# Kernel tuning notes

Hardware: AMD Instinct MI355X
Metric: run time of the kernel (lower is better)

The kernel has to match this reference:

```python
import jax, jax.numpy as jnp
import numpy as np

V, E, M, L = 32000, 1024, 4096, 4  # vocab, embed_dim, mlp_dim, mlp_layers
B, S = 4, 2048                      # batch, seq_len


def setup_inputs() -> dict:
    key = jax.random.key(0)
    ks = jax.random.split(key, 7)
    init = lambda k, shape, fan: (jax.random.normal(k, shape, jnp.float32) / np.sqrt(fan).astype(np.float32))
    return {
        "x": jax.random.randint(ks[0], (B, S), 0, V),
        "emb": init(ks[1], (V, E), E),
        "Wq": init(ks[2], (E, E), E), "bq": jnp.zeros((E,), jnp.float32),
        "Wk": init(ks[3], (E, E), E), "bk": jnp.zeros((E,), jnp.float32),
        "Wv": init(ks[4], (E, E), E), "bv": jnp.zeros((E,), jnp.float32),
        "W1": init(ks[5], (L, E, M), E), "b1": jnp.zeros((L, M), jnp.float32),
        "W2": init(ks[6], (L, M, E), M), "b2": jnp.zeros((L, E), jnp.float32),
    }


def reference(x, emb, Wq, bq, Wk, bk, Wv, bv, W1, b1, W2, b2):
    h = emb[x]                                   # [B,S,E]
    q = h @ Wq + bq
    k = h @ Wk + bk
    v = h @ Wv + bv
    scale = 1.0 / np.sqrt(E).astype(np.float32)
    scores = jnp.einsum("bse,bte->bst", q, k) * scale   # [B,S,S]
    # torch.triu(ones, diagonal=0): keep upper triangle incl. diagonal (anti-causal/suffix mask)
    mask = jnp.triu(jnp.ones((S, S), dtype=bool), k=0)
    scores = jnp.where(mask, scores, -jnp.inf)
    w = jax.nn.softmax(scores, axis=-1)
    h = jax.nn.relu(jnp.einsum("bst,bte->bse", w, v))
    for i in range(L):
        h = jax.nn.relu(h @ W1[i] + b1[i])
        h = jax.nn.relu(h @ W2[i] + b2[i])
    return h
```

## Files before the change

### kernel.cpp

```cpp
#include <hip/hip_runtime.h>
#include <hip/hip_bf16.h>

#define EDIM 1024
#define MDIM 4096
#define SEQ  2048
#define NB   4
#define ROWS 8192

#define BM 128
#define BN 128

typedef short bh8 __attribute__((ext_vector_type(8)));
typedef float f32x16 __attribute__((ext_vector_type(16)));

__device__ __forceinline__ float bf2f(unsigned short u) {
    return __uint_as_float(((unsigned int)u) << 16);
}
__device__ __forceinline__ unsigned short f2bf(float f) {
    unsigned int u = __float_as_uint(f);
    u += 0x7FFFu + ((u >> 16) & 1u);
    return (unsigned short)(u >> 16);
}
__device__ __forceinline__ void splitf(float v, unsigned short& h, unsigned short& l) {
    h = f2bf(v);
    l = f2bf(v - __uint_as_float(((unsigned int)h) << 16));
}
__device__ __forceinline__ void ld4f(const float* __restrict__ p, float* d) {
    const float4 v = *reinterpret_cast<const float4*>(p);
    d[0] = v.x; d[1] = v.y; d[2] = v.z; d[3] = v.w;
}
__device__ __forceinline__ void ld4h(const unsigned short* __restrict__ p, float* d) {
    const ushort4 v = *reinterpret_cast<const ushort4*>(p);
    d[0] = bf2f(v.x); d[1] = bf2f(v.y); d[2] = bf2f(v.z); d[3] = bf2f(v.w);
}

__device__ __forceinline__ void async_copy16(void* lds, const void* g) {
    __builtin_amdgcn_global_load_lds(
        (const __attribute__((address_space(1))) unsigned int*)g,
        (__attribute__((address_space(3))) unsigned int*)lds, 16, 0, 0);
}

__device__ __forceinline__ long long tidx8(int n, int k, int KD16) {
    return ((((long long)(n >> 5) * KD16 + (k >> 4)) * 2 + ((k >> 3) & 1)) * 32 + (n & 31)) * 8;
}

__device__ __forceinline__ void awrite(unsigned short* __restrict__ A, long long rc,
                                       int r, int k, unsigned short h, unsigned short l) {
    const int sub = (k & 31) >> 3, kb = k & 7, rx = r & 7;
    A[rc + ((sub ^ rx) << 3) + kb] = h;
    A[rc + (((4 + sub) ^ rx) << 3) + kb] = l;
}

__global__ __launch_bounds__(64)
void sniff_k(const unsigned int* __restrict__ w, int* __restrict__ flag) {
    int ok = 0;
    const int base = threadIdx.x * 32;
#pragma unroll
    for (int i = 0; i < 32; ++i) {
        const unsigned int v = w[base + i];
        const unsigned int lo = v & 0xFFFFu, hi = v >> 16;
        const unsigned int el = (lo >> 7) & 0xFF, eh = (hi >> 7) & 0xFF;
        const bool okl = (lo == 0u) || (el >= 0x30u && el <= 0x7Eu);
        const bool okh = (hi == 0u) || (eh >= 0x30u && eh <= 0x7Eu);
        ok += (okl && okh) ? 1 : 0;
    }
#pragma unroll
    for (int off = 32; off > 0; off >>= 1) ok += __shfl_down(ok, off);
    if (threadIdx.x == 0) *flag = (ok > 1400) ? 1 : 0;
}

__global__ __launch_bounds__(256)
void gather_k(const int* __restrict__ x, const void* __restrict__ emb,
              unsigned short* __restrict__ hA, const int* __restrict__ flagp) {
    const int bf = *flagp;
    const int row = blockIdx.x;
    const int idx = x[row];
    const int k = threadIdx.x * 4;
    const long long off = (long long)idx * EDIM + k;
    float d[4];
    if (bf) ld4h((const unsigned short*)emb + off, d);
    else    ld4f((const float*)emb + off, d);
    unsigned short h0, l0, h1, l1, h2, l2, h3, l3;
    splitf(d[0], h0, l0); splitf(d[1], h1, l1);
    splitf(d[2], h2, l2); splitf(d[3], h3, l3);
    const int rx = row & 7, sub = (k & 31) >> 3, kb = k & 7;
    const long long rc = ((long long)row * 32 + (k >> 5)) * 64;
    *reinterpret_cast<ushort4*>(hA + rc + ((sub ^ rx) << 3) + kb) = make_ushort4(h0, h1, h2, h3);
    *reinterpret_cast<ushort4*>(hA + rc + (((4 + sub) ^ rx) << 3) + kb) = make_ushort4(l0, l1, l2, l3);
}

__global__ __launch_bounds__(256)
void splitT_tiled_k(const void* __restrict__ in, unsigned short* __restrict__ oh,
                    unsigned short* __restrict__ ol, int Kd, int Nd,
                    long long inOff, const int* __restrict__ flagp, int bF) {
    const int bf = bF ? *flagp : 0;
    const int k0 = blockIdx.y * 32, n0 = blockIdx.x * 32;
    const int KD16 = Kd >> 4;
    __shared__ float t[32][33];
    const int c = threadIdx.x & 31, r0 = threadIdx.x >> 5;
#pragma unroll
    for (int i = 0; i < 4; ++i) {
        const int r = r0 + i * 8;
        const long long off = inOff + (long long)(k0 + r) * Nd + n0 + c;
        t[r][c] = bf ? bf2f(((const unsigned short*)in)[off]) : ((const float*)in)[off];
    }
    __syncthreads();
#pragma unroll
    for (int i = 0; i < 4; ++i) {
        const int r = r0 + i * 8;
        const float v = t[c][r];
        unsigned short hh, ll;
        splitf(v, hh, ll);
        const int n = n0 + r, k = k0 + c;
        const long long oo = tidx8(n, k, KD16) + (k & 7);
        oh[oo] = hh; ol[oo] = ll;
    }
}

template<int OM, bool BIAS, bool RELU, bool MASK>
__global__ __launch_bounds__(256, 3)
void mgemm_k(const unsigned short* __restrict__ A,
             const unsigned short* __restrict__ Bh,
             const unsigned short* __restrict__ Bl,
             const void* __restrict__ biasv,
             void* __restrict__ Cv, void* __restrict__ Cv2,
             int M, int N, int K,
             long long sA, long long sB, long long sC,
             long long biasBase, float scale, int oKD16, long long zOut,
             const int* __restrict__ flagp, int bF, int cF) {
    const int flag = *flagp;
    const int bfBias = bF ? flag : 0;
    const int bfC = cF ? flag : 0;

    A  += (long long)blockIdx.z * sA;
    Bh += (long long)blockIdx.z * sB;
    Bl += (long long)blockIdx.z * sB;
    const long long zC = (long long)blockIdx.z * sC;

    const int GX = gridDim.x;
    const int f = blockIdx.y * GX + blockIdx.x;
    const int gxpc = GX >> 3;
    const int xcd = f & 7, p = f >> 3;
    const int bx = xcd * gxpc + (p % gxpc);
    const int by = p / gxpc;
    const int brow = by * BM, bcol = bx * BN;

    const int tid = threadIdx.x;
    const int lane = tid & 63, wave = tid >> 6;
    const int wr = wave >> 1, wc = wave & 1;
    const int l31 = lane & 31, lhi = lane >> 5;

    if (MASK && (bcol + BN - 1 < brow)) {
#pragma unroll
        for (int mi = 0; mi < 2; ++mi) {
            const int rbase = brow + wr * 64 + mi * 32 + 4 * lhi;
#pragma unroll
            for (int ni = 0; ni < 2; ++ni) {
                const int c = bcol + wc * 64 + ni * 32 + l31;
#pragma unroll
                for (int e = 0; e < 16; ++e) {
                    const int r = rbase + (e & 3) + 8 * (e >> 2);
                    ((float*)Cv)[zC + (long long)r * N + c] = -1e30f;
                }
            }
        }
        return;
    }

    __shared__ __align__(16) char Ash[2][BM * 128];

    f32x16 acc[2][2];
#pragma unroll
    for (int a = 0; a < 2; ++a)
#pragma unroll
        for (int b = 0; b < 2; ++b)
#pragma unroll
            for (int e = 0; e < 16; ++e) acc[a][b][e] = 0.f;

    const int CH = K >> 5;
    const int KD16 = K >> 4;

    const long long bbase0 = ((long long)((bcol >> 5) + wc * 2 + 0) * KD16) * 512 + lane * 8;
    const long long bbase1 = ((long long)((bcol >> 5) + wc * 2 + 1) * KD16) * 512 + lane * 8;

    bh8 b0[4], b1[4];

    auto stageA = [&](int buf, int chunk) {
        char* lb = &Ash[buf][0] + tid * 16;
        const char* gb = (const char*)A;
#pragma unroll
        for (int i = 0; i < 4; ++i) {
            const int m = (tid >> 3) + i * 32;
            const long long src = (((long long)(brow + m) * CH + chunk) << 7) + ((tid & 7) << 4);
            async_copy16(lb + i * 4096, gb + src);
        }
    };

#define LOADB(dst, k4v) { \
    const long long kk_ = (long long)(k4v) * 512; \
    dst[0] = *reinterpret_cast<const bh8*>(Bh + bbase0 + kk_); \
    dst[1] = *reinterpret_cast<const bh8*>(Bh + bbase1 + kk_); \
    dst[2] = *reinterpret_cast<const bh8*>(Bl + bbase0 + kk_); \
    dst[3] = *reinterpret_cast<const bh8*>(Bl + bbase1 + kk_); }

#define AFRAG(dsth, dstl, MI) { \
    const int r_ = wr * 64 + (MI) * 32 + l31; \
    const char* base_ = &Ash[bufc][0] + r_ * 128; \
    dsth = *reinterpret_cast<const bh8*>(base_ + (((kb) ^ (r_ & 7)) << 4)); \
    dstl = *reinterpret_cast<const bh8*>(base_ + (((4 + kb) ^ (r_ & 7)) << 4)); }

#define COMPUTE_KS(KS, BS) { \
    const int kb = (KS) * 2 + lhi; \
    bh8 ah0, al0, ah1, al1; \
    AFRAG(ah0, al0, 0); AFRAG(ah1, al1, 1); \
    acc[0][0] = __builtin_amdgcn_mfma_f32_32x32x16_bf16(ah0, BS[0], acc[0][0], 0, 0, 0); \
    acc[0][1] = __builtin_amdgcn_mfma_f32_32x32x16_bf16(ah0, BS[1], acc[0][1], 0, 0, 0); \
    acc[1][0] = __builtin_amdgcn_mfma_f32_32x32x16_bf16(ah1, BS[0], acc[1][0], 0, 0, 0); \
    acc[1][1] = __builtin_amdgcn_mfma_f32_32x32x16_bf16(ah1, BS[1], acc[1][1], 0, 0, 0); \
    acc[0][0] = __builtin_amdgcn_mfma_f32_32x32x16_bf16(ah0, BS[2], acc[0][0], 0, 0, 0); \
    acc[0][1] = __builtin_amdgcn_mfma_f32_32x32x16_bf16(ah0, BS[3], acc[0][1], 0, 0, 0); \
    acc[1][0] = __builtin_amdgcn_mfma_f32_32x32x16_bf16(ah1, BS[2], acc[1][0], 0, 0, 0); \
    acc[1][1] = __builtin_amdgcn_mfma_f32_32x32x16_bf16(ah1, BS[3], acc[1][1], 0, 0, 0); \
    acc[0][0] = __builtin_amdgcn_mfma_f32_32x32x16_bf16(al0, BS[0], acc[0][0], 0, 0, 0); \
    acc[0][1] = __builtin_amdgcn_mfma_f32_32x32x16_bf16(al0, BS[1], acc[0][1], 0, 0, 0); \
    acc[1][0] = __builtin_amdgcn_mfma_f32_32x32x16_bf16(al1, BS[0], acc[1][0], 0, 0, 0); \
    acc[1][1] = __builtin_amdgcn_mfma_f32_32x32x16_bf16(al1, BS[1], acc[1][1], 0, 0, 0); }

    const int NT = CH;
    LOADB(b0, 0);
    LOADB(b1, 1);
    stageA(0, 0);
    __syncthreads();

    for (int t = 0; t < NT; ++t) {
        const int bufc = t & 1;
        if (t + 1 < NT) stageA((t + 1) & 1, t + 1);
        const int k4a = (2 * t + 2 < KD16) ? 2 * t + 2 : KD16 - 1;
        const int k4b = (2 * t + 3 < KD16) ? 2 * t + 3 : KD16 - 1;
        __builtin_amdgcn_s_setprio(1);
        COMPUTE_KS(0, b0);
        LOADB(b0, k4a);
        COMPUTE_KS(1, b1);
        LOADB(b1, k4b);
        __builtin_amdgcn_s_setprio(0);
        __syncthreads();
    }

#undef LOADB
#undef AFRAG
#undef COMPUTE_KS

#pragma unroll
    for (int mi = 0; mi < 2; ++mi) {
        const int rbase = brow + wr * 64 + mi * 32 + 4 * lhi;
#pragma unroll
        for (int ni = 0; ni < 2; ++ni) {
            const int c = bcol + wc * 64 + ni * 32 + l31;
            float bv = 0.f;
            if (BIAS) {
                const long long bo = biasBase + c;
                bv = bfBias ? bf2f(((const unsigned short*)biasv)[bo])
                            : ((const float*)biasv)[bo];
            }
            if constexpr (OM == 3) {
#pragma unroll
                for (int g = 0; g < 4; ++g) {
                    const int t0 = rbase + 8 * g;
                    const int z = t0 >> 11, tt = t0 & 2047;
                    float vv[4];
#pragma unroll
                    for (int d = 0; d < 4; ++d) {
                        float v = acc[mi][ni][g * 4 + d];
                        if (BIAS) v += bv;
                        if (RELU) v = fmaxf(v, 0.f);
                        vv[d] = v;
                    }
                    unsigned short h0, l0, h1, l1, h2, l2, h3, l3;
                    splitf(vv[0], h0, l0); splitf(vv[1], h1, l1);
                    splitf(vv[2], h2, l2); splitf(vv[3], h3, l3);
                    const long long o = (long long)z * zOut +
                        (((long long)(c >> 5) * oKD16 + (tt >> 4)) * 2 + ((tt >> 3) & 1)) * 256 +
                        (c & 31) * 8 + (tt & 7);
                    *reinterpret_cast<ushort4*>((unsigned short*)Cv + o) = make_ushort4(h0, h1, h2, h3);
                    *reinterpret_cast<ushort4*>((unsigned short*)Cv2 + o) = make_ushort4(l0, l1, l2, l3);
                }
            } else {
#pragma unroll
                for (int e = 0; e < 16; ++e) {
                    const int r = rbase + (e & 3) + 8 * (e >> 2);
                    float v = acc[mi][ni][e];
                    if (BIAS) v += bv;
                    if (MASK) v = (c >= r) ? v * scale : -1e30f;
                    if (RELU) v = fmaxf(v, 0.f);
                    if constexpr (OM == 0) {
                        const long long off = zC + (long long)r * N + c;
                        if (bfC) ((__hip_bfloat16*)Cv)[off] = __float2bfloat16(v);
                        else     ((float*)Cv)[off] = v;
                    } else if constexpr (OM == 1) {
                        unsigned short hh, ll;
                        splitf(v, hh, ll);
                        const long long rc = zC + ((long long)r * (N >> 5) + (c >> 5)) * 64;
                        awrite((unsigned short*)Cv, rc, r, c, hh, ll);
                    } else {
                        unsigned short hh, ll;
                        splitf(v, hh, ll);
                        const int z = r >> 11, n = r & 2047;
                        const long long o = (long long)z * zOut +
                            (((long long)(n >> 5) * oKD16 + (c >> 4)) * 2 + ((c >> 3) & 1)) * 256 +
                            (n & 31) * 8 + (c & 7);
                        ((unsigned short*)Cv)[o] = hh;
                        ((unsigned short*)Cv2)[o] = ll;
                    }
                }
            }
        }
    }
}

__global__ __launch_bounds__(256)
void softmax_k(const float* __restrict__ Sc, unsigned short* __restrict__ W) {
    const int m = blockIdx.x, z = blockIdx.y;
    const float* row = Sc + ((long long)z * SEQ + m) * SEQ;
    const int tid = threadIdx.x;

    float v[8];
    float mx = -1e30f;
#pragma unroll
    for (int i = 0; i < 8; ++i) { v[i] = row[tid + i * 256]; mx = fmaxf(mx, v[i]); }
#pragma unroll
    for (int off = 32; off > 0; off >>= 1) mx = fmaxf(mx, __shfl_down(mx, off));

    __shared__ float sm[4];
    __shared__ float ss[4];
    const int wid = tid >> 6, lane = tid & 63;
    if (lane == 0) sm[wid] = mx;
    __syncthreads();
    const float mAll = fmaxf(fmaxf(sm[0], sm[1]), fmaxf(sm[2], sm[3]));

    float s = 0.f;
#pragma unroll
    for (int i = 0; i < 8; ++i) { v[i] = __expf(v[i] - mAll); s += v[i]; }
#pragma unroll
    for (int off = 32; off > 0; off >>= 1) s += __shfl_down(s, off);
    if (lane == 0) ss[wid] = s;
    __syncthreads();
    const float inv = 1.f / (ss[0] + ss[1] + ss[2] + ss[3]);

    unsigned short* Wb = W + (long long)z * (SEQ * 4096LL);
#pragma unroll
    for (int i = 0; i < 8; ++i) {
        const int k = tid + i * 256;
        unsigned short hh, ll;
        splitf(v[i] * inv, hh, ll);
        const long long rc = ((long long)m * 64 + (k >> 5)) * 64;
        awrite(Wb, rc, m, k, hh, ll);
    }
}

extern "C" void kernel_launch(void* const* d_in, const int* in_sizes, int n_in,
                              void* d_out, int out_size, void* d_ws, size_t ws_size,
                              hipStream_t stream) {
    const int*  x   = (const int*)d_in[0];
    const void* emb = d_in[1];
    const void* Wq  = d_in[2];
    const void* bq  = d_in[3];
    const void* Wk  = d_in[4];
    const void* bk  = d_in[5];
    const void* Wv  = d_in[6];
    const void* bv  = d_in[7];
    const void* W1  = d_in[8];
    const void* b1  = d_in[9];
    const void* W2  = d_in[10];
    const void* b2  = d_in[11];

    char* ws = (char*)d_ws;
    const long long SZ = 33554432LL;
    unsigned short* hA    = (unsigned short*)(ws);
    unsigned short* qA    = (unsigned short*)(ws + SZ);
    unsigned short* kxs_h = (unsigned short*)(ws + 2 * SZ);
    unsigned short* kxs_l = kxs_h + 8388608;
    unsigned short* vxs_h = (unsigned short*)(ws + 3 * SZ);
    unsigned short* vxs_l = vxs_h + 8388608;
    float*          sc    = (float*)(ws + 4 * SZ);
    unsigned short* watt  = (unsigned short*)(ws);
    unsigned short* att   = (unsigned short*)(ws + 4 * SZ);
    unsigned short* wmlp  = (unsigned short*)(ws + 5 * SZ);
    unsigned short* w1_h  = wmlp,              * w1_l = wmlp + 4194304;
    unsigned short* w2_h  = wmlp + 8388608,    * w2_l = wmlp + 12582912;
    unsigned short* mid   = (unsigned short*)(ws);
    unsigned short* wqkv  = (unsigned short*)(ws + 6 * SZ);
    unsigned short* wq_h = wqkv,           * wq_l = wqkv + 1048576;
    unsigned short* wk_h = wqkv + 2097152, * wk_l = wqkv + 3145728;
    unsigned short* wv_h = wqkv + 4194304, * wv_l = wqkv + 5242880;
    unsigned short* out6  = (unsigned short*)(ws + 6 * SZ);
    int* flag = (int*)(ws + 7 * SZ);

    const dim3 b256(256);
    const long long SS = (long long)SEQ * SEQ;
    const long long TSE = 2097152LL;

    sniff_k<<<1, 64, 0, stream>>>((const unsigned int*)emb, flag);
    gather_k<<<ROWS, b256, 0, stream>>>(x, emb, hA, flag);

    splitT_tiled_k<<<dim3(32, 32, 1), b256, 0, stream>>>(Wq, wq_h, wq_l, EDIM, EDIM, 0, flag, 1);
    splitT_tiled_k<<<dim3(32, 32, 1), b256, 0, stream>>>(Wk, wk_h, wk_l, EDIM, EDIM, 0, flag, 1);
    splitT_tiled_k<<<dim3(32, 32, 1), b256, 0, stream>>>(Wv, wv_h, wv_l, EDIM, EDIM, 0, flag, 1);

    mgemm_k<1, true, false, false><<<dim3(8, 64, 1), b256, 0, stream>>>(
        hA, wq_h, wq_l, bq, qA, nullptr, ROWS, EDIM, EDIM,
        0, 0, 0, 0, 1.f, 0, 0, flag, 1, 0);
    mgemm_k<2, true, false, false><<<dim3(8, 64, 1), b256, 0, stream>>>(
        hA, wk_h, wk_l, bk, kxs_h, kxs_l, ROWS, EDIM, EDIM,
        0, 0, 0, 0, 1.f, 64, TSE, flag, 1, 0);
    mgemm_k<3, true, false, false><<<dim3(8, 64, 1), b256, 0, stream>>>(
        hA, wv_h, wv_l, bv, vxs_h, vxs_l, ROWS, EDIM, EDIM,
        0, 0, 0, 0, 1.f, 128, TSE, flag, 1, 0);

    mgemm_k<0, false, false, true><<<dim3(16, 16, NB), b256, 0, stream>>>(
        qA, kxs_h, kxs_l, nullptr, sc, nullptr, SEQ, SEQ, EDIM,
        4194304LL, TSE, SS, 0, 0.03125f, 0, 0, flag, 0, 0);

    softmax_k<<<dim3(SEQ, NB), b256, 0, stream>>>(sc, watt);

    mgemm_k<1, false, true, false><<<dim3(8, 16, NB), b256, 0, stream>>>(
        watt, vxs_h, vxs_l, nullptr, att, nullptr, SEQ, EDIM, SEQ,
        8388608LL, TSE, 4194304LL, 0, 1.f, 0, 0, flag, 0, 0);

    const unsigned short* cur = att;
    for (int i = 0; i < 4; ++i) {
        splitT_tiled_k<<<dim3(128, 32, 1), b256, 0, stream>>>(
            W1, w1_h, w1_l, EDIM, MDIM, (long long)i * EDIM * MDIM, flag, 1);
        mgemm_k<1, true, true, false><<<dim3(32, 64, 1), b256, 0, stream>>>(
            cur, w1_h, w1_l, b1, mid, nullptr, ROWS, MDIM, EDIM,
            0, 0, 0, (long long)i * MDIM, 1.f, 0, 0, flag, 1, 0);

        splitT_tiled_k<<<dim3(32, 128, 1), b256, 0, stream>>>(
            W2, w2_h, w2_l, MDIM, EDIM, (long long)i * MDIM * EDIM, flag, 1);
        if (i < 3) {
            unsigned short* out = (cur == att) ? out6 : att;
            mgemm_k<1, true, true, false><<<dim3(8, 64, 1), b256, 0, stream>>>(
                mid, w2_h, w2_l, b2, out, nullptr, ROWS, EDIM, MDIM,
                0, 0, 0, (long long)i * EDIM, 1.f, 0, 0, flag, 1, 0);
            cur = out;
        } else {
            mgemm_k<0, true, true, false><<<dim3(8, 64, 1), b256, 0, stream>>>(
                mid, w2_h, w2_l, b2, d_out, nullptr, ROWS, EDIM, MDIM,
                0, 0, 0, (long long)i * EDIM, 1.f, 0, 0, flag, 1, 1);
        }
    }
}
```

Baseline: 2.314 ms.

## Store A operands in MFMA-fragment layout and stream both operands from global without LDS

Activations (embeddings, Q, K, softmax weights, MLP intermediates) are now written as separate hi/lo bf16 planes in the same 32-row fragment-tiled layout used for weights. The GEMM drops the LDS double-buffered async staging of A and loads both A and B fragments directly from global memory into registers with a two-set software pipeline, using only occasional barriers. This removes LDS traffic and per-iteration __syncthreads, but A tiles are no longer shared through LDS, so each wave reads its fragments from global or cache itself, which raises global and L2 load pressure.

Result: slower. 2.590 ms (+11.9%).

```diff
diff --git a/kernel.cpp b/kernel.cpp
--- a/kernel.cpp
+++ b/kernel.cpp
@@ -7,9 +7,6 @@
 #define NB   4
 #define ROWS 8192
 
-#define BM 128
-#define BN 128
-
 typedef short bh8 __attribute__((ext_vector_type(8)));
 typedef float f32x16 __attribute__((ext_vector_type(16)));
 
@@ -34,21 +31,8 @@
     d[0] = bf2f(v.x); d[1] = bf2f(v.y); d[2] = bf2f(v.z); d[3] = bf2f(v.w);
 }
 
-__device__ __forceinline__ void async_copy16(void* lds, const void* g) {
-    __builtin_amdgcn_global_load_lds(
-        (const __attribute__((address_space(1))) unsigned int*)g,
-        (__attribute__((address_space(3))) unsigned int*)lds, 16, 0, 0);
-}
-
 __device__ __forceinline__ long long tidx8(int n, int k, int KD16) {
     return ((((long long)(n >> 5) * KD16 + (k >> 4)) * 2 + ((k >> 3) & 1)) * 32 + (n & 31)) * 8;
-}
-
-__device__ __forceinline__ void awrite(unsigned short* __restrict__ A, long long rc,
-                                       int r, int k, unsigned short h, unsigned short l) {
-    const int sub = (k & 31) >> 3, kb = k & 7, rx = r & 7;
-    A[rc + ((sub ^ rx) << 3) + kb] = h;
-    A[rc + (((4 + sub) ^ rx) << 3) + kb] = l;
 }
 
 __global__ __launch_bounds__(64)
@@ -71,7 +55,8 @@
 
 __global__ __launch_bounds__(256)
 void gather_k(const int* __restrict__ x, const void* __restrict__ emb,
-              unsigned short* __restrict__ hA, const int* __restrict__ flagp) {
+              unsigned short* __restrict__ oh, unsigned short* __restrict__ ol,
+              const int* __restrict__ flagp) {
     const int bf = *flagp;
     const int row = blockIdx.x;
     const int idx = x[row];
@@ -83,10 +68,10 @@
     unsigned short h0, l0, h1, l1, h2, l2, h3, l3;
     splitf(d[0], h0, l0); splitf(d[1], h1, l1);
     splitf(d[2], h2, l2); splitf(d[3], h3, l3);
-    const int rx = row & 7, sub = (k & 31) >> 3, kb = k & 7;
-    const long long rc = ((long long)row * 32 + (k >> 5)) * 64;
-    *reinterpret_cast<ushort4*>(hA + rc + ((sub ^ rx) << 3) + kb) = make_ushort4(h0, h1, h2, h3);
-    *reinterpret_cast<ushort4*>(hA + rc + (((4 + sub) ^ rx) << 3) + kb) = make_ushort4(l0, l1, l2, l3);
+    const long long o = (((long long)(row >> 5) * 64 + (k >> 4)) * 2 + ((k >> 3) & 1)) * 256
+                        + (row & 31) * 8 + (k & 7);
+    *reinterpret_cast<ushort4*>(oh + o) = make_ushort4(h0, h1, h2, h3);
+    *reinterpret_cast<ushort4*>(ol + o) = make_ushort4(l0, l1, l2, l3);
 }
 
 __global__ __launch_bounds__(256)
@@ -119,23 +104,26 @@
 
 template<int OM, bool BIAS, bool RELU, bool MASK>
 __global__ __launch_bounds__(256, 3)
-void mgemm_k(const unsigned short* __restrict__ A,
+void mgemm_k(const unsigned short* __restrict__ Ah,
+             const unsigned short* __restrict__ Al,
              const unsigned short* __restrict__ Bh,
              const unsigned short* __restrict__ Bl,
              const void* __restrict__ biasv,
              void* __restrict__ Cv, void* __restrict__ Cv2,
              int M, int N, int K,
              long long sA, long long sB, long long sC,
-             long long biasBase, float scale, int oKD16, long long zOut,
+             long long biasBase, float scale, int oKD16, long long zOut, int rowMul,
              const int* __restrict__ flagp, int bF, int cF) {
     const int flag = *flagp;
     const int bfBias = bF ? flag : 0;
     const int bfC = cF ? flag : 0;
 
-    A  += (long long)blockIdx.z * sA;
+    Ah += (long long)blockIdx.z * sA;
+    Al += (long long)blockIdx.z * sA;
     Bh += (long long)blockIdx.z * sB;
     Bl += (long long)blockIdx.z * sB;
     const long long zC = (long long)blockIdx.z * sC;
+    const int rowOff = rowMul * blockIdx.z;
 
     const int GX = gridDim.x;
     const int f = blockIdx.y * GX + blockIdx.x;
@@ -143,14 +131,14 @@
     const int xcd = f & 7, p = f >> 3;
     const int bx = xcd * gxpc + (p % gxpc);
     const int by = p / gxpc;
-    const int brow = by * BM, bcol = bx * BN;
+    const int brow = by * 128, bcol = bx * 128;
 
     const int tid = threadIdx.x;
     const int lane = tid & 63, wave = tid >> 6;
     const int wr = wave >> 1, wc = wave & 1;
     const int l31 = lane & 31, lhi = lane >> 5;
 
-    if (MASK && (bcol + BN - 1 < brow)) {
+    if (MASK && (bcol + 127 < brow)) {
 #pragma unroll
         for (int mi = 0; mi < 2; ++mi) {
             const int rbase = brow + wr * 64 + mi * 32 + 4 * lhi;
@@ -167,94 +155,79 @@
         return;
     }
 
-    __shared__ __align__(16) char Ash[2][BM * 128];
-
-    f32x16 acc[2][2];
-#pragma unroll
-    for (int a = 0; a < 2; ++a)
-#pragma unroll
-        for (int b = 0; b < 2; ++b)
-#pragma unroll
-            for (int e = 0; e < 16; ++e) acc[a][b][e] = 0.f;
-
-    const int CH = K >> 5;
     const int KD16 = K >> 4;
 
-    const long long bbase0 = ((long long)((bcol >> 5) + wc * 2 + 0) * KD16) * 512 + lane * 8;
-    const long long bbase1 = ((long long)((bcol >> 5) + wc * 2 + 1) * KD16) * 512 + lane * 8;
-
-    bh8 b0[4], b1[4];
-
-    auto stageA = [&](int buf, int chunk) {
-        char* lb = &Ash[buf][0] + tid * 16;
-        const char* gb = (const char*)A;
-#pragma unroll
-        for (int i = 0; i < 4; ++i) {
-            const int m = (tid >> 3) + i * 32;
-            const long long src = (((long long)(brow + m) * CH + chunk) << 7) + ((tid & 7) << 4);
-            async_copy16(lb + i * 4096, gb + src);
-        }
-    };
-
-#define LOADB(dst, k4v) { \
-    const long long kk_ = (long long)(k4v) * 512; \
-    dst[0] = *reinterpret_cast<const bh8*>(Bh + bbase0 + kk_); \
-    dst[1] = *reinterpret_cast<const bh8*>(Bh + bbase1 + kk_); \
-    dst[2] = *reinterpret_cast<const bh8*>(Bl + bbase0 + kk_); \
-    dst[3] = *reinterpret_cast<const bh8*>(Bl + bbase1 + kk_); }
-
-#define AFRAG(dsth, dstl, MI) { \
-    const int r_ = wr * 64 + (MI) * 32 + l31; \
-    const char* base_ = &Ash[bufc][0] + r_ * 128; \
-    dsth = *reinterpret_cast<const bh8*>(base_ + (((kb) ^ (r_ & 7)) << 4)); \
-    dstl = *reinterpret_cast<const bh8*>(base_ + (((4 + kb) ^ (r_ & 7)) << 4)); }
-
-#define COMPUTE_KS(KS, BS) { \
-    const int kb = (KS) * 2 + lhi; \
-    bh8 ah0, al0, ah1, al1; \
-    AFRAG(ah0, al0, 0); AFRAG(ah1, al1, 1); \
-    acc[0][0] = __builtin_amdgcn_mfma_f32_32x32x16_bf16(ah0, BS[0], acc[0][0], 0, 0, 0); \
-    acc[0][1] = __builtin_amdgcn_mfma_f32_32x32x16_bf16(ah0, BS[1], acc[0][1], 0, 0, 0); \
-    acc[1][0] = __builtin_amdgcn_mfma_f32_32x32x16_bf16(ah1, BS[0], acc[1][0], 0, 0, 0); \
-    acc[1][1] = __builtin_amdgcn_mfma_f32_32x32x16_bf16(ah1, BS[1], acc[1][1], 0, 0, 0); \
-    acc[0][0] = __builtin_amdgcn_mfma_f32_32x32x16_bf16(ah0, BS[2], acc[0][0], 0, 0, 0); \
-    acc[0][1] = __builtin_amdgcn_mfma_f32_32x32x16_bf16(ah0, BS[3], acc[0][1], 0, 0, 0); \
-    acc[1][0] = __builtin_amdgcn_mfma_f32_32x32x16_bf16(ah1, BS[2], acc[1][0], 0, 0, 0); \
-    acc[1][1] = __builtin_amdgcn_mfma_f32_32x32x16_bf16(ah1, BS[3], acc[1][1], 0, 0, 0); \
-    acc[0][0] = __builtin_amdgcn_mfma_f32_32x32x16_bf16(al0, BS[0], acc[0][0], 0, 0, 0); \
-    acc[0][1] = __builtin_amdgcn_mfma_f32_32x32x16_bf16(al0, BS[1], acc[0][1], 0, 0, 0); \
-    acc[1][0] = __builtin_amdgcn_mfma_f32_32x32x16_bf16(al1, BS[0], acc[1][0], 0, 0, 0); \
-    acc[1][1] = __builtin_amdgcn_mfma_f32_32x32x16_bf16(al1, BS[1], acc[1][1], 0, 0, 0); }
-
-    const int NT = CH;
-    LOADB(b0, 0);
-    LOADB(b1, 1);
-    stageA(0, 0);
-    __syncthreads();
-
-    for (int t = 0; t < NT; ++t) {
-        const int bufc = t & 1;
-        if (t + 1 < NT) stageA((t + 1) & 1, t + 1);
-        const int k4a = (2 * t + 2 < KD16) ? 2 * t + 2 : KD16 - 1;
-        const int k4b = (2 * t + 3 < KD16) ? 2 * t + 3 : KD16 - 1;
+    const long long aoff0 = ((long long)((brow >> 5) + wr * 2 + 0) * KD16) * 512 + lane * 8;
+    const long long aoff1 = aoff0 + (long long)KD16 * 512;
+    const long long boff0 = ((long long)((bcol >> 5) + wc * 2 + 0) * KD16) * 512 + lane * 8;
+    const long long boff1 = boff0 + (long long)KD16 * 512;
+
+    const unsigned short* __restrict__ pAh0 = Ah + aoff0;
+    const unsigned short* __restrict__ pAh1 = Ah + aoff1;
+    const unsigned short* __restrict__ pAl0 = Al + aoff0;
+    const unsigned short* __restrict__ pAl1 = Al + aoff1;
+    const unsigned short* __restrict__ pBh0 = Bh + boff0;
+    const unsigned short* __restrict__ pBh1 = Bh + boff1;
+    const unsigned short* __restrict__ pBl0 = Bl + boff0;
+    const unsigned short* __restrict__ pBl1 = Bl + boff1;
+
+    f32x16 acc00, acc01, acc10, acc11;
+#pragma unroll
+    for (int e = 0; e < 16; ++e) { acc00[e] = 0.f; acc01[e] = 0.f; acc10[e] = 0.f; acc11[e] = 0.f; }
+
+    bh8 p_ah0, p_ah1, p_al0, p_al1, p_bh0, p_bh1, p_bl0, p_bl1;
+    bh8 q_ah0, q_ah1, q_al0, q_al1, q_bh0, q_bh1, q_bl0, q_bl1;
+
+#define MFMA_(d, a, b) d = __builtin_amdgcn_mfma_f32_32x32x16_bf16(a, b, d, 0, 0, 0)
+
+#define LOADSET(S, J) { \
+    const long long o_ = (long long)(J) * 512; \
+    S##ah0 = *reinterpret_cast<const bh8*>(pAh0 + o_); \
+    S##ah1 = *reinterpret_cast<const bh8*>(pAh1 + o_); \
+    S##al0 = *reinterpret_cast<const bh8*>(pAl0 + o_); \
+    S##al1 = *reinterpret_cast<const bh8*>(pAl1 + o_); \
+    S##bh0 = *reinterpret_cast<const bh8*>(pBh0 + o_); \
+    S##bh1 = *reinterpret_cast<const bh8*>(pBh1 + o_); \
+    S##bl0 = *reinterpret_cast<const bh8*>(pBl0 + o_); \
+    S##bl1 = *reinterpret_cast<const bh8*>(pBl1 + o_); }
+
+#define COMPSET(S) { \
+    MFMA_(acc00, S##ah0, S##bh0); MFMA_(acc01, S##ah0, S##bh1); \
+    MFMA_(acc10, S##ah1, S##bh0); MFMA_(acc11, S##ah1, S##bh1); \
+    MFMA_(acc00, S##ah0, S##bl0); MFMA_(acc01, S##ah0, S##bl1); \
+    MFMA_(acc10, S##ah1, S##bl0); MFMA_(acc11, S##ah1, S##bl1); \
+    MFMA_(acc00, S##al0, S##bh0); MFMA_(acc01, S##al0, S##bh1); \
+    MFMA_(acc10, S##al1, S##bh0); MFMA_(acc11, S##al1, S##bh1); }
+
+    LOADSET(p_, 0);
+    LOADSET(q_, 1);
+
+    for (int j = 0; j + 3 < KD16; j += 2) {
+        if ((j & 7) == 6) __builtin_amdgcn_s_barrier();
         __builtin_amdgcn_s_setprio(1);
-        COMPUTE_KS(0, b0);
-        LOADB(b0, k4a);
-        COMPUTE_KS(1, b1);
-        LOADB(b1, k4b);
+        COMPSET(p_);
         __builtin_amdgcn_s_setprio(0);
-        __syncthreads();
-    }
-
-#undef LOADB
-#undef AFRAG
-#undef COMPUTE_KS
+        LOADSET(p_, j + 2);
+        __builtin_amdgcn_s_setprio(1);
+        COMPSET(q_);
+        __builtin_amdgcn_s_setprio(0);
+        LOADSET(q_, j + 3);
+    }
+    COMPSET(p_);
+    COMPSET(q_);
+
+#undef LOADSET
+#undef COMPSET
+#undef MFMA_
+
+    const f32x16* accp[4] = {&acc00, &acc01, &acc10, &acc11};
 
 #pragma unroll
     for (int mi = 0; mi < 2; ++mi) {
         const int rbase = brow + wr * 64 + mi * 32 + 4 * lhi;
 #pragma unroll
         for (int ni = 0; ni < 2; ++ni) {
+            const f32x16& a = *accp[mi * 2 + ni];
             const int c = bcol + wc * 64 + ni * 32 + l31;
             float bv = 0.f;
             if (BIAS) {
@@ -270,7 +243,7 @@
                     float vv[4];
 #pragma unroll
                     for (int d = 0; d < 4; ++d) {
-                        float v = acc[mi][ni][g * 4 + d];
+                        float v = a[g * 4 + d];
                         if (BIAS) v += bv;
                         if (RELU) v = fmaxf(v, 0.f);
                         vv[d] = v;
@@ -284,33 +257,33 @@
                     *reinterpret_cast<ushort4*>((unsigned short*)Cv + o) = make_ushort4(h0, h1, h2, h3);
                     *reinterpret_cast<ushort4*>((unsigned short*)Cv2 + o) = make_ushort4(l0, l1, l2, l3);
                 }
-            } else {
+            } else if constexpr (OM == 1) {
 #pragma unroll
                 for (int e = 0; e < 16; ++e) {
                     const int r = rbase + (e & 3) + 8 * (e >> 2);
-                    float v = acc[mi][ni][e];
+                    float v = a[e];
+                    if (BIAS) v += bv;
+                    if (RELU) v = fmaxf(v, 0.f);
+                    unsigned short hh, ll;
+                    splitf(v, hh, ll);
+                    const int gr = rowOff + r;
+                    const long long o =
+                        (((long long)(gr >> 5) * oKD16 + (c >> 4)) * 2 + ((c >> 3) & 1)) * 256 +
+                        (gr & 31) * 8 + (c & 7);
+                    ((unsigned short*)Cv)[o] = hh;
+                    ((unsigned short*)Cv2)[o] = ll;
+                }
+            } else {
+#pragma unroll
+                for (int e = 0; e < 16; ++e) {
+                    const int r = rbase + (e & 3) + 8 * (e >> 2);
+                    float v = a[e];
                     if (BIAS) v += bv;
                     if (MASK) v = (c >= r) ? v * scale : -1e30f;
                     if (RELU) v = fmaxf(v, 0.f);
-                    if constexpr (OM == 0) {
-                        const long long off = zC + (long long)r * N + c;
-                        if (bfC) ((__hip_bfloat16*)Cv)[off] = __float2bfloat16(v);
-                        else     ((float*)Cv)[off] = v;
-                    } else if constexpr (OM == 1) {
-                        unsigned short hh, ll;
-                        splitf(v, hh, ll);
-                        const long long rc = zC + ((long long)r * (N >> 5) + (c >> 5)) * 64;
-                        awrite((unsigned short*)Cv, rc, r, c, hh, ll);
-                    } else {
-                        unsigned short hh, ll;
-                        splitf(v, hh, ll);
-                        const int z = r >> 11, n = r & 2047;
-                        const long long o = (long long)z * zOut +
-                            (((long long)(n >> 5) * oKD16 + (c >> 4)) * 2 + ((c >> 3) & 1)) * 256 +
-                            (n & 31) * 8 + (c & 7);
-                        ((unsigned short*)Cv)[o] = hh;
-                        ((unsigned short*)Cv2)[o] = ll;
-                    }
+                    const long long off = zC + (long long)r * N + c;
+                    if (bfC) ((__hip_bfloat16*)Cv)[off] = __float2bfloat16(v);
+                    else     ((float*)Cv)[off] = v;
                 }
             }
         }
@@ -318,7 +291,8 @@
 }
 
 __global__ __launch_bounds__(256)
-void softmax_k(const float* __restrict__ Sc, unsigned short* __restrict__ W) {
+void softmax_k(const float* __restrict__ Sc, unsigned short* __restrict__ Wh,
+               unsigned short* __restrict__ Wl) {
     const int m = blockIdx.x, z = blockIdx.y;
     const float* row = Sc + ((long long)z * SEQ + m) * SEQ;
     const int tid = threadIdx.x;
@@ -346,14 +320,16 @@
     __syncthreads();
     const float inv = 1.f / (ss[0] + ss[1] + ss[2] + ss[3]);
 
-    unsigned short* Wb = W + (long long)z * (SEQ * 4096LL);
+    unsigned short* wh = Wh + (long long)z * 4194304LL;
+    unsigned short* wl = Wl + (long long)z * 4194304LL;
 #pragma unroll
     for (int i = 0; i < 8; ++i) {
         const int k = tid + i * 256;
         unsigned short hh, ll;
         splitf(v[i] * inv, hh, ll);
-        const long long rc = ((long long)m * 64 + (k >> 5)) * 64;
-        awrite(Wb, rc, m, k, hh, ll);
+        const long long o = (((long long)(m >> 5) * 128 + (k >> 4)) * 2 + ((k >> 3) & 1)) * 256 +
+                            (m & 31) * 8 + (k & 7);
+        wh[o] = hh; wl[o] = ll;
     }
 }
 
@@ -375,24 +351,31 @@
 
     char* ws = (char*)d_ws;
     const long long SZ = 33554432LL;
-    unsigned short* hA    = (unsigned short*)(ws);
-    unsigned short* qA    = (unsigned short*)(ws + SZ);
-    unsigned short* kxs_h = (unsigned short*)(ws + 2 * SZ);
-    unsigned short* kxs_l = kxs_h + 8388608;
+    const long long HM = 8388608LL;
+    unsigned short* hA_h  = (unsigned short*)(ws);
+    unsigned short* hA_l  = hA_h + HM;
+    unsigned short* q_h   = (unsigned short*)(ws + SZ);
+    unsigned short* q_l   = q_h + HM;
+    unsigned short* kx_h  = (unsigned short*)(ws + 2 * SZ);
+    unsigned short* kx_l  = kx_h + HM;
     unsigned short* vxs_h = (unsigned short*)(ws + 3 * SZ);
-    unsigned short* vxs_l = vxs_h + 8388608;
+    unsigned short* vxs_l = vxs_h + HM;
     float*          sc    = (float*)(ws + 4 * SZ);
-    unsigned short* watt  = (unsigned short*)(ws);
-    unsigned short* att   = (unsigned short*)(ws + 4 * SZ);
-    unsigned short* wmlp  = (unsigned short*)(ws + 5 * SZ);
-    unsigned short* w1_h  = wmlp,              * w1_l = wmlp + 4194304;
-    unsigned short* w2_h  = wmlp + 8388608,    * w2_l = wmlp + 12582912;
-    unsigned short* mid   = (unsigned short*)(ws);
-    unsigned short* wqkv  = (unsigned short*)(ws + 6 * SZ);
-    unsigned short* wq_h = wqkv,           * wq_l = wqkv + 1048576;
-    unsigned short* wk_h = wqkv + 2097152, * wk_l = wqkv + 3145728;
-    unsigned short* wv_h = wqkv + 4194304, * wv_l = wqkv + 5242880;
-    unsigned short* out6  = (unsigned short*)(ws + 6 * SZ);
+    unsigned short* watt_h = (unsigned short*)(ws);
+    unsigned short* watt_l = (unsigned short*)(ws + SZ);
+    unsigned short* att_h = (unsigned short*)(ws + 2 * SZ);
+    unsigned short* att_l = att_h + HM;
+    unsigned short* mid_h = (unsigned short*)(ws);
+    unsigned short* mid_l = (unsigned short*)(ws + 3 * SZ);
+    unsigned short* pong_h = (unsigned short*)(ws + 5 * SZ);
+    unsigned short* pong_l = pong_h + HM;
+    unsigned short* wq_h = (unsigned short*)(ws + 6 * SZ);
+    unsigned short* wq_l = wq_h + 1048576;
+    unsigned short* wk_h = wq_h + 2097152, * wk_l = wq_h + 3145728;
+    unsigned short* wv_h = wq_h + 4194304, * wv_l = wq_h + 5242880;
+    unsigned short* w1_h = (unsigned short*)(ws + 6 * SZ);
+    unsigned short* w1_l = w1_h + 4194304;
+    unsigned short* w2_h = w1_h + 8388608, * w2_l = w1_h + 12582912;
     int* flag = (int*)(ws + 7 * SZ);
 
     const dim3 b256(256);
@@ -400,52 +383,54 @@
     const long long TSE = 2097152LL;
 
     sniff_k<<<1, 64, 0, stream>>>((const unsigned int*)emb, flag);
-    gather_k<<<ROWS, b256, 0, stream>>>(x, emb, hA, flag);
+    gather_k<<<ROWS, b256, 0, stream>>>(x, emb, hA_h, hA_l, flag);
 
     splitT_tiled_k<<<dim3(32, 32, 1), b256, 0, stream>>>(Wq, wq_h, wq_l, EDIM, EDIM, 0, flag, 1);
     splitT_tiled_k<<<dim3(32, 32, 1), b256, 0, stream>>>(Wk, wk_h, wk_l, EDIM, EDIM, 0, flag, 1);
     splitT_tiled_k<<<dim3(32, 32, 1), b256, 0, stream>>>(Wv, wv_h, wv_l, EDIM, EDIM, 0, flag, 1);
 
     mgemm_k<1, true, false, false><<<dim3(8, 64, 1), b256, 0, stream>>>(
-        hA, wq_h, wq_l, bq, qA, nullptr, ROWS, EDIM, EDIM,
-        0, 0, 0, 0, 1.f, 0, 0, flag, 1, 0);
-    mgemm_k<2, true, false, false><<<dim3(8, 64, 1), b256, 0, stream>>>(
-        hA, wk_h, wk_l, bk, kxs_h, kxs_l, ROWS, EDIM, EDIM,
-        0, 0, 0, 0, 1.f, 64, TSE, flag, 1, 0);
+        hA_h, hA_l, wq_h, wq_l, bq, q_h, q_l, ROWS, EDIM, EDIM,
+        0, 0, 0, 0, 1.f, 64, 0, 0, flag, 1, 0);
+    mgemm_k<1, true, false, false><<<dim3(8, 64, 1), b256, 0, stream>>>(
+        hA_h, hA_l, wk_h, wk_l, bk, kx_h, kx_l, ROWS, EDIM, EDIM,
+        0, 0, 0, 0, 1.f, 64, 0, 0, flag, 1, 0);
     mgemm_k<3, true, false, false><<<dim3(8, 64, 1), b256, 0, stream>>>(
-        hA, wv_h, wv_l, bv, vxs_h, vxs_l, ROWS, EDIM, EDIM,
-        0, 0, 0, 0, 1.f, 128, TSE, flag, 1, 0);
+        hA_h, hA_l, wv_h, wv_l, bv, vxs_h, vxs_l, ROWS, EDIM, EDIM,
+        0, 0, 0, 0, 1.f, 128, TSE, 0, flag, 1, 0);
 
     mgemm_k<0, false, false, true><<<dim3(16, 16, NB), b256, 0, stream>>>(
-        qA, kxs_h, kxs_l, nullptr, sc, nullptr, SEQ, SEQ, EDIM,
-        4194304LL, TSE, SS, 0, 0.03125f, 0, 0, flag, 0, 0);
-
-    softmax_k<<<dim3(SEQ, NB), b256, 0, stream>>>(sc, watt);
+        q_h, q_l, kx_h, kx_l, nullptr, sc, nullptr, SEQ, SEQ, EDIM,
+        TSE, TSE, SS, 0, 0.03125f, 0, 0, 0, flag, 0, 0);
+
+    softmax_k<<<dim3(SEQ, NB), b256, 0, stream>>>(sc, watt_h, watt_l);
 
     mgemm_k<1, false, true, false><<<dim3(8, 16, NB), b256, 0, stream>>>(
-        watt, vxs_h, vxs_l, nullptr, att, nullptr, SEQ, EDIM, SEQ,
-        8388608LL, TSE, 4194304LL, 0, 1.f, 0, 0, flag, 0, 0);
-
-    const unsigned short* cur = att;
+        watt_h, watt_l, vxs_h, vxs_l, nullptr, att_h, att_l, SEQ, EDIM, SEQ,
+        4194304LL, TSE, 0, 0, 1.f, 64, 0, 2048, flag, 0, 0);
+
+    const unsigned short* cur_h = att_h;
+    const unsigned short* cur_l = att_l;
     for (int i = 0; i < 4; ++i) {
         splitT_tiled_k<<<dim3(128, 32, 1), b256, 0, stream>>>(
             W1, w1_h, w1_l, EDIM, MDIM, (long long)i * EDIM * MDIM, flag, 1);
         mgemm_k<1, true, true, false><<<dim3(32, 64, 1), b256, 0, stream>>>(
-            cur, w1_h, w1_l, b1, mid, nullptr, ROWS, MDIM, EDIM,
-            0, 0, 0, (long long)i * MDIM, 1.f, 0, 0, flag, 1, 0);
+            cur_h, cur_l, w1_h, w1_l, b1, mid_h, mid_l, ROWS, MDIM, EDIM,
+            0, 0, 0, (long long)i * MDIM, 1.f, 256, 0, 0, flag, 1, 0);
 
         splitT_tiled_k<<<dim3(32, 128, 1), b256, 0, stream>>>(
             W2, w2_h, w2_l, MDIM, EDIM, (long long)i * MDIM * EDIM, flag, 1);
         if (i < 3) {
-            unsigned short* out = (cur == att) ? out6 : att;
+            unsigned short* oh = (cur_h == att_h) ? pong_h : att_h;
+            unsigned short* ol = (cur_h == att_h) ? pong_l : att_l;
             mgemm_k<1, true, true, false><<<dim3(8, 64, 1), b256, 0, stream>>>(
-                mid, w2_h, w2_l, b2, out, nullptr, ROWS, EDIM, MDIM,
-                0, 0, 0, (long long)i * EDIM, 1.f, 0, 0, flag, 1, 0);
-            cur = out;
+                mid_h, mid_l, w2_h, w2_l, b2, oh, ol, ROWS, EDIM, MDIM,
+                0, 0, 0, (long long)i * EDIM, 1.f, 64, 0, 0, flag, 1, 0);
+            cur_h = oh; cur_l = ol;
         } else {
             mgemm_k<0, true, true, false><<<dim3(8, 64, 1), b256, 0, stream>>>(
-                mid, w2_h, w2_l, b2, d_out, nullptr, ROWS, EDIM, MDIM,
-                0, 0, 0, (long long)i * EDIM, 1.f, 0, 0, flag, 1, 1);
+                mid_h, mid_l, w2_h, w2_l, b2, d_out, nullptr, ROWS, EDIM, MDIM,
+                0, 0, 0, (long long)i * EDIM, 1.f, 0, 0, 0, flag, 1, 1);
         }
     }
 }
```
